# Kernel optimization log

Hardware: AMD Instinct MI355X
Metric: run time of the kernel (lower is better)

## Reference

```python
import jax, jax.numpy as jnp
import numpy as np

B, N, C = 2, 16384, 3        # clouds, points per cloud, feature dim
M, K = 2048, 64              # num_out_points (FPS centers), max_num_neighbors
R = 0.2                      # ball-query radius
H1, H2, HOUT = 64, 64, 128   # local_nn MLP widths


def setup_inputs() -> dict:
    key = jax.random.key(0)
    ks = jax.random.split(key, 8)
    return {
        "x": jax.random.normal(ks[0], (B, N, C), jnp.float32),
        "pos": jax.random.uniform(ks[1], (B, N, 3), jnp.float32),
        "W1": jax.random.normal(ks[2], (C + 3, H1), jnp.float32) * 0.1,
        "b1": jnp.zeros((H1,), jnp.float32),
        "W2": jax.random.normal(ks[3], (H1, H2), jnp.float32) * 0.1,
        "b2": jnp.zeros((H2,), jnp.float32),
        "W3": jax.random.normal(ks[4], (H2, HOUT), jnp.float32) * 0.1,
        "b3": jnp.zeros((HOUT,), jnp.float32),
    }


def _fps(pos):
    """Iterative farthest point sampling for one cloud. pos: [N,3] -> idx [M]."""
    mind = jnp.sum((pos - pos[0]) ** 2, axis=-1)  # start from point 0

    def step(mind, _):
        nxt = jnp.argmax(mind)
        mind = jnp.minimum(mind, jnp.sum((pos - pos[nxt]) ** 2, axis=-1))
        return mind, nxt.astype(jnp.int32)

    _, idx = jax.lax.scan(step, mind, None, length=M - 1)
    return jnp.concatenate([jnp.zeros((1,), jnp.int32), idx])


def reference(x, pos, W1, b1, W2, b2, W3, b3):
    # 1) FPS: pick M centers per cloud (vectorized over batch)
    idx = jax.vmap(_fps)(pos)                                   # [B, M]
    centers = jnp.take_along_axis(pos, idx[..., None], axis=1)  # [B, M, 3]

    # 2) ball query: up to K neighbors within radius R of each center
    d2 = jnp.sum((centers[:, :, None, :] - pos[:, None, :, :]) ** 2, axis=-1)  # [B,M,N]
    masked = jnp.where(d2 <= R * R, d2, jnp.inf)
    neg_top, nbr = jax.lax.top_k(-masked, K)   # K nearest within radius; nbr [B,M,K]
    valid = neg_top > -jnp.inf                 # in-radius mask

    # 3) gather -> local MLP -> max scatter (PointNetConv, aggr='max')
    gather = jax.vmap(lambda arr, i: arr[i])   # per-cloud fancy gather
    pos_j = gather(pos, nbr)                   # [B, M, K, 3]
    x_j = gather(x, nbr)                       # [B, M, K, C]
    rel = pos_j - centers[:, :, None, :]
    feat = jnp.concatenate([x_j, rel], axis=-1)          # [B, M, K, C+3]
    h = jax.nn.relu(feat @ W1 + b1)
    h = jax.nn.relu(h @ W2 + b2)
    h = h @ W3 + b3                                       # [B, M, K, HOUT]
    h = jnp.where(valid[..., None], h, -jnp.inf)
    out = jnp.max(h, axis=2)                              # [B, M, HOUT]
    out = jnp.where(jnp.isfinite(out), out, 0.0)          # empty-neighborhood guard
    return out, centers
```

## Files before the change

### kernel.cpp

```cpp
#include <hip/hip_runtime.h>
#include <cstdint>

#define NPT   16384
#define BATCH 2
#define MOUT  2048
#define KNBR  64
#define CAP   2048
#define FPS_T 1024
#define PPT   (NPT / FPS_T)
#define NW    (FPS_T / 64)

#define R2_F32 0.039999999105930328f

__device__ __forceinline__ float d2_exact(float ax, float ay, float az,
                                          float bx, float by, float bz) {
  float dx = __fsub_rn(ax, bx);
  float dy = __fsub_rn(ay, by);
  float dz = __fsub_rn(az, bz);
  return __fadd_rn(__fadd_rn(__fmul_rn(dx, dx), __fmul_rn(dy, dy)),
                   __fmul_rn(dz, dz));
}

__global__ void prep_kernel(const float* __restrict__ W1,
                            const float* __restrict__ W2,
                            const float* __restrict__ W3,
                            float* __restrict__ ws) {
  int t = threadIdx.x + blockIdx.x * blockDim.x;
  int stride = blockDim.x * gridDim.x;
  for (int idx = t; idx < 64 * 6; idx += stride) {
    int j = idx / 6, i = idx - j * 6;
    ws[idx] = W1[i * 64 + j];
  }
  for (int idx = t; idx < 64 * 64; idx += stride) {
    int j = idx >> 6, i = idx & 63;
    ws[384 + idx] = W2[i * 64 + j];
  }
  for (int idx = t; idx < 128 * 64; idx += stride) {
    int j = idx >> 6, i = idx & 63;
    ws[4480 + idx] = W3[i * 128 + j];
  }
}

__device__ __forceinline__ int morton3_8(int x, int y, int z) {
  int c = 0;
#pragma unroll
  for (int k = 0; k < 3; ++k)
    c |= (((x >> k) & 1) << (3 * k)) | (((y >> k) & 1) << (3 * k + 1)) |
         (((z >> k) & 1) << (3 * k + 2));
  return c;
}

__global__ __launch_bounds__(512) void bin_kernel(
    const float* __restrict__ pos, float* __restrict__ sx,
    float* __restrict__ sy, float* __restrict__ sz, int* __restrict__ soi) {
  const int b = blockIdx.x;
  const int t = threadIdx.x;
  const float* __restrict__ P = pos + (size_t)b * NPT * 3;

  __shared__ int hist[512];
  __shared__ int scan[512];
  __shared__ unsigned short cid[NPT];

  hist[t] = 0;
  __syncthreads();

  for (int p = 0; p < 32; ++p) {
    int g = t + p * 512;
    float x = P[g * 3 + 0], y = P[g * 3 + 1], z = P[g * 3 + 2];
    int ix = (int)(x * 8.0f); ix = ix < 0 ? 0 : (ix > 7 ? 7 : ix);
    int iy = (int)(y * 8.0f); iy = iy < 0 ? 0 : (iy > 7 ? 7 : iy);
    int iz = (int)(z * 8.0f); iz = iz < 0 ? 0 : (iz > 7 ? 7 : iz);
    int c = morton3_8(ix, iy, iz);
    cid[g] = (unsigned short)c;
    atomicAdd(&hist[c], 1);
  }
  __syncthreads();

  int cnt = hist[t];
  int v = cnt;
  scan[t] = v;
  __syncthreads();
  for (int off = 1; off < 512; off <<= 1) {
    int add = (t >= off) ? scan[t - off] : 0;
    __syncthreads();
    v += add;
    scan[t] = v;
    __syncthreads();
  }
  hist[t] = scan[t] - cnt;
  __syncthreads();

  for (int p = 0; p < 32; ++p) {
    int g = t + p * 512;
    int c = cid[g];
    int dst = atomicAdd(&hist[c], 1);
    sx[b * NPT + dst] = P[g * 3 + 0];
    sy[b * NPT + dst] = P[g * 3 + 1];
    sz[b * NPT + dst] = P[g * 3 + 2];
    soi[b * NPT + dst] = g;
  }
}

__global__ __launch_bounds__(FPS_T) void fps_kernel(
    const float* __restrict__ pos, const float* __restrict__ sx,
    const float* __restrict__ sy, const float* __restrict__ sz,
    const int* __restrict__ soi, float* __restrict__ centers) {
  const int b = blockIdx.x;
  const int t = threadIdx.x;
  const int lane = t & 63;
  const int wid = t >> 6;
  const float* __restrict__ P = pos + (size_t)b * NPT * 3;
  float* __restrict__ Cout = centers + (size_t)b * MOUT * 3;

  float px[PPT], py[PPT], pz[PPT], mind[PPT];
  int oid[PPT];
  const int base = b * NPT + t * PPT;
#pragma unroll
  for (int p = 0; p < PPT; ++p) {
    px[p] = sx[base + p];
    py[p] = sy[base + p];
    pz[p] = sz[base + p];
    oid[p] = soi[base + p];
  }

  float lox = px[0], hix = px[0], loy = py[0], hiy = py[0], loz = pz[0], hiz = pz[0];
#pragma unroll
  for (int p = 1; p < PPT; ++p) {
    lox = fminf(lox, px[p]); hix = fmaxf(hix, px[p]);
    loy = fminf(loy, py[p]); hiy = fmaxf(hiy, py[p]);
    loz = fminf(loz, pz[p]); hiz = fmaxf(hiz, pz[p]);
  }

  __shared__ float wmax[NW];
  __shared__ float qs[3];
  __shared__ int owner;

  float qx = P[0], qy = P[1], qz = P[2];
  if (t == 0) {
    Cout[0] = qx; Cout[1] = qy; Cout[2] = qz;
    owner = 0x7fffffff;
  }

  float t0 = -1.0f, t1 = -1.0f;
#pragma unroll
  for (int p = 0; p < PPT; ++p) {
    float d2 = d2_exact(px[p], py[p], pz[p], qx, qy, qz);
    mind[p] = d2;
    if (p & 1) t1 = fmaxf(t1, d2); else t0 = fmaxf(t0, d2);
  }
  float tm = fmaxf(t0, t1);

  for (int s = 1; s < MOUT; ++s) {
    float v = tm;
#pragma unroll
    for (int d = 1; d < 64; d <<= 1) v = fmaxf(v, __shfl_xor(v, d, 64));
    if (lane == 0) wmax[wid] = v;
    __syncthreads();
    float gv = wmax[0];
#pragma unroll
    for (int w = 1; w < NW; ++w) gv = fmaxf(gv, wmax[w]);

    if (tm == gv) {
      int cand = 0x7fffffff;
#pragma unroll
      for (int p = 0; p < PPT; ++p)
        if (mind[p] == gv) cand = min(cand, (oid[p] << 14) | (t << 4) | p);
      atomicMin(&owner, cand);
    }
    __syncthreads();

    int w = owner;
    if (t == ((w >> 4) & 1023)) {
      int slot = w & 15;
#pragma unroll
      for (int p = 0; p < PPT; ++p)
        if (p == slot) {
          qs[0] = px[p]; qs[1] = py[p]; qs[2] = pz[p];
          Cout[s * 3 + 0] = px[p];
          Cout[s * 3 + 1] = py[p];
          Cout[s * 3 + 2] = pz[p];
        }
    }
    __syncthreads();
    qx = qs[0]; qy = qs[1]; qz = qs[2];
    if (t == 0) owner = 0x7fffffff;

    float ddx = fmaxf(fmaxf(lox - qx, qx - hix), 0.0f);
    float ddy = fmaxf(fmaxf(loy - qy, qy - hiy), 0.0f);
    float ddz = fmaxf(fmaxf(loz - qz, qz - hiz), 0.0f);
    float dmin2 = ddx * ddx + ddy * ddy + ddz * ddz;
    if (dmin2 <= tm * 1.0001f) {
      float u0 = -1.0f, u1 = -1.0f;
#pragma unroll
      for (int p = 0; p < PPT; ++p) {
        float d2 = d2_exact(px[p], py[p], pz[p], qx, qy, qz);
        float m = fminf(mind[p], d2);
        mind[p] = m;
        if (p & 1) u1 = fmaxf(u1, m); else u0 = fmaxf(u0, m);
      }
      tm = fmaxf(u0, u1);
    }
  }
}

__global__ __launch_bounds__(256) void ballq_kernel(
    const float* __restrict__ pos, const float* __restrict__ centers,
    int* __restrict__ nbr, int* __restrict__ ncnt) {
  const int bm = blockIdx.x;
  const int b = bm >> 11;
  const int t = threadIdx.x;

  __shared__ unsigned long long keys[CAP];
  __shared__ int cnt;
  if (t == 0) cnt = 0;
  __syncthreads();

  const float cx = centers[(size_t)bm * 3 + 0];
  const float cy = centers[(size_t)bm * 3 + 1];
  const float cz = centers[(size_t)bm * 3 + 2];
  const float* __restrict__ P = pos + (size_t)b * NPT * 3;

  for (int g = t; g < NPT; g += 256) {
    float d2 = d2_exact(cx, cy, cz, P[g * 3 + 0], P[g * 3 + 1], P[g * 3 + 2]);
    if (d2 <= R2_F32) {
      int s = atomicAdd(&cnt, 1);
      if (s < CAP)
        keys[s] = ((unsigned long long)__float_as_uint(d2) << 32) |
                  (unsigned long long)(unsigned)g;
    }
  }
  __syncthreads();

  int C = cnt; if (C > CAP) C = CAP;
  int P2 = 64; while (P2 < C) P2 <<= 1;
  for (int i = C + t; i < P2; i += 256) keys[i] = ~0ULL;
  __syncthreads();

  for (int k = 2; k <= P2; k <<= 1) {
    for (int j = k >> 1; j > 0; j >>= 1) {
      for (int i = t; i < P2; i += 256) {
        int ixj = i ^ j;
        if (ixj > i) {
          unsigned long long a = keys[i], c = keys[ixj];
          bool up = ((i & k) == 0);
          if ((a > c) == up) { keys[i] = c; keys[ixj] = a; }
        }
      }
      __syncthreads();
    }
  }

  if (t < KNBR) {
    int v = (t < C) ? (int)(unsigned)(keys[t] & 0xFFFFFFFFull) : -1;
    nbr[(size_t)bm * KNBR + t] = v;
  }
  if (t == 0) ncnt[bm] = (C < KNBR) ? C : KNBR;
}

__global__ __launch_bounds__(256) void mlp_kernel(
    const float* __restrict__ x, const float* __restrict__ pos,
    const float* __restrict__ centers, const int* __restrict__ nbr,
    const int* __restrict__ ncnt, const float* __restrict__ wsw,
    const float* __restrict__ b1, const float* __restrict__ b2,
    const float* __restrict__ b3, float* __restrict__ out) {
  const int lane = threadIdx.x & 63;
  const int bm = blockIdx.x * 4 + (threadIdx.x >> 6);
  const int b = bm >> 11;

  const float* __restrict__ w1t = wsw;
  const float* __restrict__ w2t = wsw + 384;
  const float* __restrict__ w3t = wsw + 4480;

  const int cnt = ncnt[bm];
  const bool valid = lane < cnt;
  int gr = nbr[(size_t)bm * KNBR + lane];
  int g = valid ? gr : 0;

  const float cx = centers[(size_t)bm * 3 + 0];
  const float cy = centers[(size_t)bm * 3 + 1];
  const float cz = centers[(size_t)bm * 3 + 2];
  const float* __restrict__ Pb = pos + (size_t)b * NPT * 3;
  const float* __restrict__ Xb = x + (size_t)b * NPT * 3;

  float f0 = Xb[g * 3 + 0], f1 = Xb[g * 3 + 1], f2 = Xb[g * 3 + 2];
  float f3 = Pb[g * 3 + 0] - cx, f4 = Pb[g * 3 + 1] - cy, f5 = Pb[g * 3 + 2] - cz;

  float h1[64];
#pragma unroll
  for (int j = 0; j < 64; ++j) {
    float a = b1[j];
    a = fmaf(f0, w1t[j * 6 + 0], a);
    a = fmaf(f1, w1t[j * 6 + 1], a);
    a = fmaf(f2, w1t[j * 6 + 2], a);
    a = fmaf(f3, w1t[j * 6 + 3], a);
    a = fmaf(f4, w1t[j * 6 + 4], a);
    a = fmaf(f5, w1t[j * 6 + 5], a);
    h1[j] = fmaxf(a, 0.0f);
  }

  float h2[64];
#pragma unroll
  for (int j = 0; j < 64; ++j) {
    float a = b2[j];
#pragma unroll
    for (int i = 0; i < 64; ++i) a = fmaf(h1[i], w2t[j * 64 + i], a);
    h2[j] = fmaxf(a, 0.0f);
  }

  float* __restrict__ O = out + (size_t)bm * 128;
#pragma unroll
  for (int j = 0; j < 128; ++j) {
    float a = b3[j];
#pragma unroll
    for (int i = 0; i < 64; ++i) a = fmaf(h2[i], w3t[j * 64 + i], a);
    float v = valid ? a : -INFINITY;
#pragma unroll
    for (int d = 1; d < 64; d <<= 1) v = fmaxf(v, __shfl_xor(v, d, 64));
    if (v == -INFINITY) v = 0.0f;
    if (lane == 0) O[j] = v;
  }
}

extern "C" void kernel_launch(void* const* d_in, const int* in_sizes, int n_in,
                              void* d_out, int out_size, void* d_ws,
                              size_t ws_size, hipStream_t stream) {
  const float* x   = (const float*)d_in[0];
  const float* pos = (const float*)d_in[1];
  const float* W1  = (const float*)d_in[2];
  const float* b1  = (const float*)d_in[3];
  const float* W2  = (const float*)d_in[4];
  const float* b2  = (const float*)d_in[5];
  const float* W3  = (const float*)d_in[6];
  const float* b3  = (const float*)d_in[7];

  float* out     = (float*)d_out;
  float* centers = out + (size_t)BATCH * MOUT * 128;

  char* wsb = (char*)d_ws;
  float* wsw = (float*)d_ws;
  float* sx = (float*)(wsb + 51200);
  float* sy = (float*)(wsb + 182272);
  float* sz = (float*)(wsb + 313344);
  int*   soi = (int*)(wsb + 444416);
  int*   nbr = (int*)(wsb + 51200);
  int*   ncnt = (int*)(wsb + 51200 + (size_t)BATCH * MOUT * KNBR * 4);

  prep_kernel<<<32, 256, 0, stream>>>(W1, W2, W3, wsw);
  bin_kernel<<<BATCH, 512, 0, stream>>>(pos, sx, sy, sz, soi);
  fps_kernel<<<BATCH, FPS_T, 0, stream>>>(pos, sx, sy, sz, soi, centers);
  ballq_kernel<<<BATCH * MOUT, 256, 0, stream>>>(pos, centers, nbr, ncnt);
  mlp_kernel<<<BATCH * MOUT / 4, 256, 0, stream>>>(x, pos, centers, nbr, ncnt,
                                                   wsw, b1, b2, b3, out);
}
```

Measured before the change: 3.383 ms.

## Cut FPS loop to one barrier per step with packed atomics and DPP reductions

The FPS iteration now publishes the winning point's coordinates through 64-bit atomicMin on packed (candidate index, coordinate) keys held in double-buffered shared slots. This removes the second barrier and the owner-broadcast step in each of the 2047 sequential iterations. Wave-wide max reductions now use DPP row ops plus readlane instead of shuffle loops, in both FPS and the MLP max-pool, and the per-thread max chains are split four ways. The cost is three extra 64-bit LDS atomics from the winning thread, and the result depends on the DPP control encodings being correct for wave64.

```diff
diff --git a/kernel.cpp b/kernel.cpp
--- a/kernel.cpp
+++ b/kernel.cpp
@@ -19,6 +19,23 @@
   float dz = __fsub_rn(az, bz);
   return __fadd_rn(__fadd_rn(__fmul_rn(dx, dx), __fmul_rn(dy, dy)),
                    __fmul_rn(dz, dz));
+}
+
+template <int CTRL, int ROW>
+__device__ __forceinline__ float dpp_max_step(float x) {
+  int v = __float_as_int(x);
+  int p = __builtin_amdgcn_update_dpp(v, v, CTRL, ROW, 0xF, false);
+  return fmaxf(x, __int_as_float(p));
+}
+
+__device__ __forceinline__ float wave_max64(float x) {
+  x = dpp_max_step<0xB1, 0xF>(x);
+  x = dpp_max_step<0x4E, 0xF>(x);
+  x = dpp_max_step<0x141, 0xF>(x);
+  x = dpp_max_step<0x140, 0xF>(x);
+  x = dpp_max_step<0x142, 0xA>(x);
+  x = dpp_max_step<0x143, 0xC>(x);
+  return __int_as_float(__builtin_amdgcn_readlane(__float_as_int(x), 63));
 }
 
 __global__ void prep_kernel(const float* __restrict__ W1,
@@ -132,73 +149,83 @@
   }
 
   __shared__ float wmax[NW];
-  __shared__ float qs[3];
-  __shared__ int owner;
+  __shared__ unsigned long long qpack[2][3];
 
   float qx = P[0], qy = P[1], qz = P[2];
   if (t == 0) {
     Cout[0] = qx; Cout[1] = qy; Cout[2] = qz;
-    owner = 0x7fffffff;
-  }
-
-  float t0 = -1.0f, t1 = -1.0f;
+    qpack[0][0] = qpack[0][1] = qpack[0][2] = ~0ULL;
+    qpack[1][0] = qpack[1][1] = qpack[1][2] = ~0ULL;
+  }
+
+  float t0_ = -1.0f, t1_ = -1.0f, t2_ = -1.0f, t3_ = -1.0f;
 #pragma unroll
   for (int p = 0; p < PPT; ++p) {
     float d2 = d2_exact(px[p], py[p], pz[p], qx, qy, qz);
     mind[p] = d2;
-    if (p & 1) t1 = fmaxf(t1, d2); else t0 = fmaxf(t0, d2);
-  }
-  float tm = fmaxf(t0, t1);
+    if ((p & 3) == 0) t0_ = fmaxf(t0_, d2);
+    else if ((p & 3) == 1) t1_ = fmaxf(t1_, d2);
+    else if ((p & 3) == 2) t2_ = fmaxf(t2_, d2);
+    else t3_ = fmaxf(t3_, d2);
+  }
+  float tm = fmaxf(fmaxf(t0_, t1_), fmaxf(t2_, t3_));
 
   for (int s = 1; s < MOUT; ++s) {
-    float v = tm;
-#pragma unroll
-    for (int d = 1; d < 64; d <<= 1) v = fmaxf(v, __shfl_xor(v, d, 64));
-    if (lane == 0) wmax[wid] = v;
+    const int B = s & 1;
+    float wv = wave_max64(tm);
+    if (lane == 0) wmax[wid] = wv;
     __syncthreads();
-    float gv = wmax[0];
-#pragma unroll
-    for (int w = 1; w < NW; ++w) gv = fmaxf(gv, wmax[w]);
+    float g01 = fmaxf(wmax[0], wmax[1]),   g23 = fmaxf(wmax[2], wmax[3]);
+    float g45 = fmaxf(wmax[4], wmax[5]),   g67 = fmaxf(wmax[6], wmax[7]);
+    float g89 = fmaxf(wmax[8], wmax[9]),   gab = fmaxf(wmax[10], wmax[11]);
+    float gcd = fmaxf(wmax[12], wmax[13]), gef = fmaxf(wmax[14], wmax[15]);
+    float gv = fmaxf(fmaxf(fmaxf(g01, g23), fmaxf(g45, g67)),
+                     fmaxf(fmaxf(g89, gab), fmaxf(gcd, gef)));
 
     if (tm == gv) {
       int cand = 0x7fffffff;
 #pragma unroll
       for (int p = 0; p < PPT; ++p)
         if (mind[p] == gv) cand = min(cand, (oid[p] << 14) | (t << 4) | p);
-      atomicMin(&owner, cand);
+      unsigned long long hi = ((unsigned long long)(unsigned)cand) << 32;
+#pragma unroll
+      for (int p = 0; p < PPT; ++p)
+        if ((cand & 15) == p) {
+          atomicMin(&qpack[B][0], hi | (unsigned long long)__float_as_uint(px[p]));
+          atomicMin(&qpack[B][1], hi | (unsigned long long)__float_as_uint(py[p]));
+          atomicMin(&qpack[B][2], hi | (unsigned long long)__float_as_uint(pz[p]));
+        }
     }
     __syncthreads();
 
-    int w = owner;
-    if (t == ((w >> 4) & 1023)) {
-      int slot = w & 15;
-#pragma unroll
-      for (int p = 0; p < PPT; ++p)
-        if (p == slot) {
-          qs[0] = px[p]; qs[1] = py[p]; qs[2] = pz[p];
-          Cout[s * 3 + 0] = px[p];
-          Cout[s * 3 + 1] = py[p];
-          Cout[s * 3 + 2] = pz[p];
-        }
-    }
-    __syncthreads();
-    qx = qs[0]; qy = qs[1]; qz = qs[2];
-    if (t == 0) owner = 0x7fffffff;
+    unsigned long long wx = qpack[B][0];
+    unsigned long long wy = qpack[B][1];
+    unsigned long long wz = qpack[B][2];
+    qx = __uint_as_float((unsigned)wx);
+    qy = __uint_as_float((unsigned)wy);
+    qz = __uint_as_float((unsigned)wz);
+    if (t == 0) {
+      Cout[s * 3 + 0] = qx; Cout[s * 3 + 1] = qy; Cout[s * 3 + 2] = qz;
+      qpack[B ^ 1][0] = ~0ULL; qpack[B ^ 1][1] = ~0ULL; qpack[B ^ 1][2] = ~0ULL;
+    }
 
     float ddx = fmaxf(fmaxf(lox - qx, qx - hix), 0.0f);
     float ddy = fmaxf(fmaxf(loy - qy, qy - hiy), 0.0f);
     float ddz = fmaxf(fmaxf(loz - qz, qz - hiz), 0.0f);
     float dmin2 = ddx * ddx + ddy * ddy + ddz * ddz;
     if (dmin2 <= tm * 1.0001f) {
-      float u0 = -1.0f, u1 = -1.0f;
+      float u0 = -1.0f, u1 = -1.0f, u2 = -1.0f, u3 = -1.0f;
 #pragma unroll
       for (int p = 0; p < PPT; ++p) {
         float d2 = d2_exact(px[p], py[p], pz[p], qx, qy, qz);
         float m = fminf(mind[p], d2);
         mind[p] = m;
-        if (p & 1) u1 = fmaxf(u1, m); else u0 = fmaxf(u0, m);
+        if ((p & 3) == 0) u0 = fmaxf(u0, m);
+        else if ((p & 3) == 1) u1 = fmaxf(u1, m);
+        else if ((p & 3) == 2) u2 = fmaxf(u2, m);
+        else u3 = fmaxf(u3, m);
       }
-      tm = fmaxf(u0, u1);
+      tm = fmaxf(fmaxf(u0, u1), fmaxf(u2, u3));
     }
   }
 }
@@ -314,8 +341,7 @@
 #pragma unroll
     for (int i = 0; i < 64; ++i) a = fmaf(h2[i], w3t[j * 64 + i], a);
     float v = valid ? a : -INFINITY;
-#pragma unroll
-    for (int d = 1; d < 64; d <<= 1) v = fmaxf(v, __shfl_xor(v, d, 64));
+    v = wave_max64(v);
     if (v == -INFINITY) v = 0.0f;
     if (lane == 0) O[j] = v;
   }
```

New measurement: 3.392 ms. Within noise of the previous version (+0.3%).
